# Performance work log

Measured on AMD Instinct MI355X. Metric: run time of the kernel, lower is better.

## Reference

```python
import jax, jax.numpy as jnp
import numpy as np
import math

B, T, C, H = 16384, 64, 48, 48


def setup_inputs() -> dict:
    key = jax.random.key(0)
    kx, kq, kk, kv = jax.random.split(key, 4)
    return {
        "x": jax.random.normal(kx, (B, T, C), dtype=jnp.float32),
        "Wq": jax.random.normal(kq, (C, H), dtype=jnp.float32) * 0.02,
        "Wk": jax.random.normal(kk, (C, H), dtype=jnp.float32) * 0.02,
        "Wv": jax.random.normal(kv, (C, H), dtype=jnp.float32) * 0.02,
    }


def reference(x, Wq, Wk, Wv):
    # x: [B, T, C]; projections (Linear with bias=False): [B, T, H]
    q = x @ Wq
    k = x @ Wk
    v = x @ Wv
    scale = 1.0 / math.sqrt(H)
    # scores: [B, T, T]
    wei = jnp.einsum("bth,bsh->bts", q, k) * scale
    causal = jnp.tril(jnp.ones((T, T), dtype=bool))  # tril mask, T==BLOCK_SIZE
    wei = jnp.where(causal, wei, -jnp.inf)
    wei = jax.nn.softmax(wei, axis=-1)
    # dropout is identity in eval mode
    return jnp.einsum("bts,bsh->bth", wei, v)
```

## Files before the change

kernel.cpp:

```cpp
#include <hip/hip_runtime.h>
#include <math.h>

typedef __bf16 bf16x8 __attribute__((ext_vector_type(8)));
typedef float f32x4 __attribute__((ext_vector_type(4)));
typedef unsigned short u16;

__device__ __forceinline__ u16 f2b(float f) {
  unsigned u = __builtin_bit_cast(unsigned, f);
  u = (u + 0x7fffu + ((u >> 16) & 1u)) >> 16;
  return (u16)u;
}

__device__ __forceinline__ f32x4 mfma16(bf16x8 a, bf16x8 b, f32x4 c) {
  return __builtin_amdgcn_mfma_f32_16x16x32_bf16(a, b, c, 0, 0, 0);
}

__device__ __forceinline__ int sw(int r, int c) {
  return (r << 6) + ((((c >> 3) ^ r) & 7) << 3) + (c & 7);
}
__device__ __forceinline__ int swc(int r, int ch) {
  return (r << 6) + (((ch ^ r) & 7) << 3);
}

__global__ __launch_bounds__(256) void head_prep(const float* __restrict__ Wq,
                                                 const float* __restrict__ Wk,
                                                 const float* __restrict__ Wv,
                                                 u16* __restrict__ ws) {
  __shared__ float wq[2304], wk[2304], wv[2304];
  const float scale = 0.14433756729740643f;
  for (int i = threadIdx.x; i < 2304; i += 256) {
    wq[i] = Wq[i];
    wk[i] = Wk[i];
    wv[i] = Wv[i];
  }
  __syncthreads();
  for (int idx = threadIdx.x; idx < 96 * 64; idx += 256) {
    int r = idx >> 6, c = idx & 63;
    float v = 0.f;
    if (c < 48) {
      if (r < 48) {
        float a = 0.f;
        for (int h = 0; h < 48; ++h) a += wq[c * 48 + h] * wk[r * 48 + h];
        v = a * scale;
      } else {
        v = wv[c * 48 + (r - 48)];
      }
    }
    ws[sw(r, c)] = f2b(v);
  }
}

__global__ __launch_bounds__(256, 6) void head_main(const float* __restrict__ x,
                                                    const u16* __restrict__ wimg,
                                                    float* __restrict__ out) {
  __shared__ u16 lds[208 * 64];
  u16* const R0 = lds;
  u16* const X  = lds + 96 * 64;
  u16* const VT = lds + 160 * 64;

  const int tid  = threadIdx.x;
  const int lane = tid & 63;
  const int w    = tid >> 6;
  const int qd   = lane >> 4;
  const int col  = lane & 15;
  const long b   = blockIdx.x;

  {
    const uint4* src = (const uint4*)wimg;
    uint4* dst = (uint4*)lds;
    dst[tid]       = src[tid];
    dst[tid + 256] = src[tid + 256];
    dst[tid + 512] = src[tid + 512];
  }
  {
    const float* xb = x + b * 3072;
#pragma unroll
    for (int it = 0; it < 3; ++it) {
      int flat = tid * 4 + it * 1024;
      float4 v = *(const float4*)(xb + flat);
      int row = flat / 48;
      int c0  = flat % 48;
      ushort4 pk;
      pk.x = f2b(v.x); pk.y = f2b(v.y); pk.z = f2b(v.z); pk.w = f2b(v.w);
      *(ushort4*)(X + sw(row, c0)) = pk;
    }
    int zr = tid >> 2;
    int zq = tid & 3;
    ushort4 z = {0, 0, 0, 0};
    *(ushort4*)(X + swc(zr, 6 + (zq >> 1)) + (zq & 1) * 4) = z;
  }
  __syncthreads();

  f32x4 aq[3];
  {
    const int ar = 16 * w + col;
    const bf16x8 xa0 = *(const bf16x8*)(X + swc(ar, qd));
    const bf16x8 xa1 = *(const bf16x8*)(X + swc(ar, qd + 4));
    const u16* WM = R0;
    const u16* WV = R0 + 48 * 64;
#pragma unroll
    for (int n = 0; n < 3; ++n) {
      const int br = 16 * n + col;
      const int b0 = swc(br, qd);
      const int b1 = swc(br, qd + 4);
      f32x4 av = {0.f, 0.f, 0.f, 0.f};
      av = mfma16(xa0, *(const bf16x8*)(WV + b0), av);
      av = mfma16(xa1, *(const bf16x8*)(WV + b1), av);
      f32x4 a = {0.f, 0.f, 0.f, 0.f};
      a = mfma16(xa0, *(const bf16x8*)(WM + b0), a);
      a = mfma16(xa1, *(const bf16x8*)(WM + b1), a);
      aq[n] = a;
      ushort4 pv;
      pv.x = f2b(av[0]); pv.y = f2b(av[1]); pv.z = f2b(av[2]); pv.w = f2b(av[3]);
      *(ushort4*)(VT + sw(16 * n + col, 16 * w + qd * 4)) = pv;
    }
  }
  __syncthreads();

#pragma unroll
  for (int n = 0; n < 3; ++n)
#pragma unroll
    for (int i = 0; i < 4; ++i)
      R0[sw(16 * w + qd * 4 + i, 16 * n + col)] = f2b(aq[n][i]);
  __threadfence_block();

  float sv[4][4];
  {
    const int ar = 16 * w + col;
    const bf16x8 qa0 = *(const bf16x8*)(R0 + swc(ar, qd));
    const bf16x8 qa1 = *(const bf16x8*)(R0 + swc(ar, qd + 4));
#pragma unroll
    for (int st = 0; st < 4; ++st) {
      const int br = 16 * st + col;
      f32x4 a = {0.f, 0.f, 0.f, 0.f};
      a = mfma16(qa0, *(const bf16x8*)(X + swc(br, qd)), a);
      a = mfma16(qa1, *(const bf16x8*)(X + swc(br, qd + 4)), a);
#pragma unroll
      for (int i = 0; i < 4; ++i) sv[st][i] = a[i];
    }
  }

  float m4[4] = {-INFINITY, -INFINITY, -INFINITY, -INFINITY};
#pragma unroll
  for (int st = 0; st < 4; ++st)
#pragma unroll
    for (int i = 0; i < 4; ++i) {
      int tg = 16 * w + qd * 4 + i;
      int sg = 16 * st + col;
      float v = (sg <= tg) ? sv[st][i] : -INFINITY;
      sv[st][i] = v;
      m4[i] = fmaxf(m4[i], v);
    }
#pragma unroll
  for (int d = 1; d < 16; d <<= 1)
#pragma unroll
    for (int i = 0; i < 4; ++i) m4[i] = fmaxf(m4[i], __shfl_xor(m4[i], d, 64));
  float l4[4] = {0.f, 0.f, 0.f, 0.f};
#pragma unroll
  for (int st = 0; st < 4; ++st)
#pragma unroll
    for (int i = 0; i < 4; ++i) {
      float p = __expf(sv[st][i] - m4[i]);
      sv[st][i] = p;
      l4[i] += p;
    }
#pragma unroll
  for (int d = 1; d < 16; d <<= 1)
#pragma unroll
    for (int i = 0; i < 4; ++i) l4[i] += __shfl_xor(l4[i], d, 64);

  __syncthreads();

#pragma unroll
  for (int st = 0; st < 4; ++st)
#pragma unroll
    for (int i = 0; i < 4; ++i)
      X[sw(16 * w + qd * 4 + i, 16 * st + col)] = f2b(sv[st][i]);
  __threadfence_block();

  f32x4 o0 = {0.f, 0.f, 0.f, 0.f}, o1 = o0, o2 = o0;
  {
    const int pr = 16 * w + col;
#pragma unroll
    for (int kt = 0; kt < 2; ++kt) {
      const int ch = qd + 4 * kt;
      bf16x8 pa = *(const bf16x8*)(X + swc(pr, ch));
      o0 = mfma16(pa, *(const bf16x8*)(VT + swc(0  + col, ch)), o0);
      o1 = mfma16(pa, *(const bf16x8*)(VT + swc(16 + col, ch)), o1);
      o2 = mfma16(pa, *(const bf16x8*)(VT + swc(32 + col, ch)), o2);
    }
  }
  float rl[4];
#pragma unroll
  for (int i = 0; i < 4; ++i) rl[i] = __builtin_amdgcn_rcpf(l4[i]);

  float* ob = out + b * 3072 + (16 * w + qd * 4) * 48 + col;
#pragma unroll
  for (int i = 0; i < 4; ++i) {
    ob[i * 48 +  0] = o0[i] * rl[i];
    ob[i * 48 + 16] = o1[i] * rl[i];
    ob[i * 48 + 32] = o2[i] * rl[i];
  }
}

extern "C" void kernel_launch(void* const* d_in, const int* in_sizes, int n_in,
                              void* d_out, int out_size, void* d_ws, size_t ws_size,
                              hipStream_t stream) {
  const float* x  = (const float*)d_in[0];
  const float* Wq = (const float*)d_in[1];
  const float* Wk = (const float*)d_in[2];
  const float* Wv = (const float*)d_in[3];
  u16* wimg = (u16*)d_ws;
  head_prep<<<1, 256, 0, stream>>>(Wq, Wk, Wv, wimg);
  head_main<<<16384, 256, 0, stream>>>(x, wimg, (float*)d_out);
}
```

Baseline: 340.6 us.

## Process several batches per block with register prefetch of next x tile

Each block now handles NB=8 consecutive batch elements in a loop. The weight image is loaded into LDS once per block instead of once per batch element, and the next batch's x tile is prefetched into registers while the current one is computed. This is meant to amortise the weight load and launch overhead and to hide global-load latency. In exchange, each block uses more LDS because Q and X get separate buffers, occupancy is lowered to 4 blocks per SM, and the grid shrinks to 2048 blocks.

Result: slower. 357.3 us (+4.9%).

```diff
diff --git a/kernel.cpp b/kernel.cpp
--- a/kernel.cpp
+++ b/kernel.cpp
@@ -4,6 +4,8 @@
 typedef __bf16 bf16x8 __attribute__((ext_vector_type(8)));
 typedef float f32x4 __attribute__((ext_vector_type(4)));
 typedef unsigned short u16;
+
+#define NB 8
 
 __device__ __forceinline__ u16 f2b(float f) {
   unsigned u = __builtin_bit_cast(unsigned, f);
@@ -50,20 +52,21 @@
   }
 }
 
-__global__ __launch_bounds__(256, 6) void head_main(const float* __restrict__ x,
+__global__ __launch_bounds__(256, 4) void head_main(const float* __restrict__ x,
                                                     const u16* __restrict__ wimg,
                                                     float* __restrict__ out) {
-  __shared__ u16 lds[208 * 64];
-  u16* const R0 = lds;
-  u16* const X  = lds + 96 * 64;
-  u16* const VT = lds + 160 * 64;
+  __shared__ u16 lds[272 * 64];
+  u16* const W  = lds;
+  u16* const QM = lds + 96 * 64;
+  u16* const X  = lds + 160 * 64;
+  u16* const VT = lds + 224 * 64;
 
   const int tid  = threadIdx.x;
   const int lane = tid & 63;
   const int w    = tid >> 6;
   const int qd   = lane >> 4;
   const int col  = lane & 15;
-  const long b   = blockIdx.x;
+  const long b0  = (long)blockIdx.x * NB;
 
   {
     const uint4* src = (const uint4*)wimg;
@@ -73,133 +76,155 @@
     dst[tid + 512] = src[tid + 512];
   }
   {
-    const float* xb = x + b * 3072;
-#pragma unroll
-    for (int it = 0; it < 3; ++it) {
-      int flat = tid * 4 + it * 1024;
-      float4 v = *(const float4*)(xb + flat);
-      int row = flat / 48;
-      int c0  = flat % 48;
-      ushort4 pk;
-      pk.x = f2b(v.x); pk.y = f2b(v.y); pk.z = f2b(v.z); pk.w = f2b(v.w);
-      *(ushort4*)(X + sw(row, c0)) = pk;
-    }
-    int zr = tid >> 2;
-    int zq = tid & 3;
     ushort4 z = {0, 0, 0, 0};
-    *(ushort4*)(X + swc(zr, 6 + (zq >> 1)) + (zq & 1) * 4) = z;
-  }
-  __syncthreads();
-
-  f32x4 aq[3];
-  {
-    const int ar = 16 * w + col;
-    const bf16x8 xa0 = *(const bf16x8*)(X + swc(ar, qd));
-    const bf16x8 xa1 = *(const bf16x8*)(X + swc(ar, qd + 4));
-    const u16* WM = R0;
-    const u16* WV = R0 + 48 * 64;
-#pragma unroll
-    for (int n = 0; n < 3; ++n) {
-      const int br = 16 * n + col;
-      const int b0 = swc(br, qd);
-      const int b1 = swc(br, qd + 4);
-      f32x4 av = {0.f, 0.f, 0.f, 0.f};
-      av = mfma16(xa0, *(const bf16x8*)(WV + b0), av);
-      av = mfma16(xa1, *(const bf16x8*)(WV + b1), av);
-      f32x4 a = {0.f, 0.f, 0.f, 0.f};
-      a = mfma16(xa0, *(const bf16x8*)(WM + b0), a);
-      a = mfma16(xa1, *(const bf16x8*)(WM + b1), a);
-      aq[n] = a;
-      ushort4 pv;
-      pv.x = f2b(av[0]); pv.y = f2b(av[1]); pv.z = f2b(av[2]); pv.w = f2b(av[3]);
-      *(ushort4*)(VT + sw(16 * n + col, 16 * w + qd * 4)) = pv;
-    }
-  }
-  __syncthreads();
-
-#pragma unroll
-  for (int n = 0; n < 3; ++n)
-#pragma unroll
-    for (int i = 0; i < 4; ++i)
-      R0[sw(16 * w + qd * 4 + i, 16 * n + col)] = f2b(aq[n][i]);
-  __threadfence_block();
-
-  float sv[4][4];
-  {
-    const int ar = 16 * w + col;
-    const bf16x8 qa0 = *(const bf16x8*)(R0 + swc(ar, qd));
-    const bf16x8 qa1 = *(const bf16x8*)(R0 + swc(ar, qd + 4));
-#pragma unroll
-    for (int st = 0; st < 4; ++st) {
-      const int br = 16 * st + col;
-      f32x4 a = {0.f, 0.f, 0.f, 0.f};
-      a = mfma16(qa0, *(const bf16x8*)(X + swc(br, qd)), a);
-      a = mfma16(qa1, *(const bf16x8*)(X + swc(br, qd + 4)), a);
-#pragma unroll
-      for (int i = 0; i < 4; ++i) sv[st][i] = a[i];
-    }
-  }
-
-  float m4[4] = {-INFINITY, -INFINITY, -INFINITY, -INFINITY};
-#pragma unroll
-  for (int st = 0; st < 4; ++st)
-#pragma unroll
-    for (int i = 0; i < 4; ++i) {
-      int tg = 16 * w + qd * 4 + i;
-      int sg = 16 * st + col;
-      float v = (sg <= tg) ? sv[st][i] : -INFINITY;
-      sv[st][i] = v;
-      m4[i] = fmaxf(m4[i], v);
-    }
-#pragma unroll
-  for (int d = 1; d < 16; d <<= 1)
-#pragma unroll
-    for (int i = 0; i < 4; ++i) m4[i] = fmaxf(m4[i], __shfl_xor(m4[i], d, 64));
-  float l4[4] = {0.f, 0.f, 0.f, 0.f};
-#pragma unroll
-  for (int st = 0; st < 4; ++st)
-#pragma unroll
-    for (int i = 0; i < 4; ++i) {
-      float p = __expf(sv[st][i] - m4[i]);
-      sv[st][i] = p;
-      l4[i] += p;
-    }
-#pragma unroll
-  for (int d = 1; d < 16; d <<= 1)
-#pragma unroll
-    for (int i = 0; i < 4; ++i) l4[i] += __shfl_xor(l4[i], d, 64);
-
-  __syncthreads();
-
-#pragma unroll
-  for (int st = 0; st < 4; ++st)
-#pragma unroll
-    for (int i = 0; i < 4; ++i)
-      X[sw(16 * w + qd * 4 + i, 16 * st + col)] = f2b(sv[st][i]);
-  __threadfence_block();
-
-  f32x4 o0 = {0.f, 0.f, 0.f, 0.f}, o1 = o0, o2 = o0;
-  {
-    const int pr = 16 * w + col;
-#pragma unroll
-    for (int kt = 0; kt < 2; ++kt) {
-      const int ch = qd + 4 * kt;
-      bf16x8 pa = *(const bf16x8*)(X + swc(pr, ch));
-      o0 = mfma16(pa, *(const bf16x8*)(VT + swc(0  + col, ch)), o0);
-      o1 = mfma16(pa, *(const bf16x8*)(VT + swc(16 + col, ch)), o1);
-      o2 = mfma16(pa, *(const bf16x8*)(VT + swc(32 + col, ch)), o2);
-    }
-  }
-  float rl[4];
-#pragma unroll
-  for (int i = 0; i < 4; ++i) rl[i] = __builtin_amdgcn_rcpf(l4[i]);
-
-  float* ob = out + b * 3072 + (16 * w + qd * 4) * 48 + col;
-#pragma unroll
-  for (int i = 0; i < 4; ++i) {
-    ob[i * 48 +  0] = o0[i] * rl[i];
-    ob[i * 48 + 16] = o1[i] * rl[i];
-    ob[i * 48 + 32] = o2[i] * rl[i];
+    int zr = tid >> 2, zq = tid & 3;
+    *(ushort4*)(QM + swc(zr, 6 + (zq >> 1)) + (zq & 1) * 4) = z;
+  }
+
+  const int f0 = tid * 4, f1 = f0 + 1024, f2 = f0 + 2048;
+  const int xw0 = sw(f0 / 48, f0 % 48);
+  const int xw1 = sw(f1 / 48, f1 % 48);
+  const int xw2 = sw(f2 / 48, f2 % 48);
+  const int zr = tid >> 2, zq = tid & 3;
+  const int zpad = swc(zr, 6 + (zq >> 1)) + (zq & 1) * 4;
+
+  const int ar = 16 * w + col;
+  const int a0 = swc(ar, qd), a1 = swc(ar, qd + 4);
+
+  const float* xb = x + b0 * 3072;
+  float4 p0 = *(const float4*)(xb + f0);
+  float4 p1 = *(const float4*)(xb + f1);
+  float4 p2 = *(const float4*)(xb + f2);
+
+  for (int i = 0; i < NB; ++i) {
+    if (i > 0) __syncthreads();
+
+    {
+      ushort4 s;
+      s.x = f2b(p0.x); s.y = f2b(p0.y); s.z = f2b(p0.z); s.w = f2b(p0.w);
+      *(ushort4*)(X + xw0) = s;
+      s.x = f2b(p1.x); s.y = f2b(p1.y); s.z = f2b(p1.z); s.w = f2b(p1.w);
+      *(ushort4*)(X + xw1) = s;
+      s.x = f2b(p2.x); s.y = f2b(p2.y); s.z = f2b(p2.z); s.w = f2b(p2.w);
+      *(ushort4*)(X + xw2) = s;
+      ushort4 z = {0, 0, 0, 0};
+      *(ushort4*)(X + zpad) = z;
+    }
+    {
+      const long bn = b0 + ((i < NB - 1) ? i + 1 : i);
+      const float* xn = x + bn * 3072;
+      p0 = *(const float4*)(xn + f0);
+      p1 = *(const float4*)(xn + f1);
+      p2 = *(const float4*)(xn + f2);
+    }
+    __syncthreads();
+
+    f32x4 aq[3];
+    {
+      const bf16x8 xa0 = *(const bf16x8*)(X + a0);
+      const bf16x8 xa1 = *(const bf16x8*)(X + a1);
+      const u16* WM = W;
+      const u16* WV = W + 48 * 64;
+#pragma unroll
+      for (int n = 0; n < 3; ++n) {
+        const int br = 16 * n + col;
+        const int c0 = swc(br, qd), c1 = swc(br, qd + 4);
+        f32x4 av = {0.f, 0.f, 0.f, 0.f};
+        av = mfma16(xa0, *(const bf16x8*)(WV + c0), av);
+        av = mfma16(xa1, *(const bf16x8*)(WV + c1), av);
+        f32x4 a = {0.f, 0.f, 0.f, 0.f};
+        a = mfma16(xa0, *(const bf16x8*)(WM + c0), a);
+        a = mfma16(xa1, *(const bf16x8*)(WM + c1), a);
+        aq[n] = a;
+        ushort4 pv;
+        pv.x = f2b(av[0]); pv.y = f2b(av[1]); pv.z = f2b(av[2]); pv.w = f2b(av[3]);
+        *(ushort4*)(VT + sw(16 * n + col, 16 * w + qd * 4)) = pv;
+      }
+    }
+
+#pragma unroll
+    for (int n = 0; n < 3; ++n)
+#pragma unroll
+      for (int j = 0; j < 4; ++j)
+        QM[sw(16 * w + qd * 4 + j, 16 * n + col)] = f2b(aq[n][j]);
+    __threadfence_block();
+
+    float sv[4][4];
+    {
+      const bf16x8 qa0 = *(const bf16x8*)(QM + a0);
+      const bf16x8 qa1 = *(const bf16x8*)(QM + a1);
+#pragma unroll
+      for (int st = 0; st < 4; ++st) {
+        const int br = 16 * st + col;
+        f32x4 a = {0.f, 0.f, 0.f, 0.f};
+        a = mfma16(qa0, *(const bf16x8*)(X + swc(br, qd)), a);
+        a = mfma16(qa1, *(const bf16x8*)(X + swc(br, qd + 4)), a);
+#pragma unroll
+        for (int j = 0; j < 4; ++j) sv[st][j] = a[j];
+      }
+    }
+
+    float m4[4] = {-INFINITY, -INFINITY, -INFINITY, -INFINITY};
+#pragma unroll
+    for (int st = 0; st < 4; ++st)
+#pragma unroll
+      for (int j = 0; j < 4; ++j) {
+        int tg = 16 * w + qd * 4 + j;
+        int sg = 16 * st + col;
+        float v = (sg <= tg) ? sv[st][j] : -INFINITY;
+        sv[st][j] = v;
+        m4[j] = fmaxf(m4[j], v);
+      }
+#pragma unroll
+    for (int d = 1; d < 16; d <<= 1)
+#pragma unroll
+      for (int j = 0; j < 4; ++j) m4[j] = fmaxf(m4[j], __shfl_xor(m4[j], d, 64));
+    float l4[4] = {0.f, 0.f, 0.f, 0.f};
+#pragma unroll
+    for (int st = 0; st < 4; ++st)
+#pragma unroll
+      for (int j = 0; j < 4; ++j) {
+        float p = __expf(sv[st][j] - m4[j]);
+        sv[st][j] = p;
+        l4[j] += p;
+      }
+#pragma unroll
+    for (int d = 1; d < 16; d <<= 1)
+#pragma unroll
+      for (int j = 0; j < 4; ++j) l4[j] += __shfl_xor(l4[j], d, 64);
+
+    __syncthreads();
+
+#pragma unroll
+    for (int st = 0; st < 4; ++st)
+#pragma unroll
+      for (int j = 0; j < 4; ++j)
+        X[sw(16 * w + qd * 4 + j, 16 * st + col)] = f2b(sv[st][j]);
+    __threadfence_block();
+
+    f32x4 o0 = {0.f, 0.f, 0.f, 0.f}, o1 = o0, o2 = o0;
+    {
+      const int pr = 16 * w + col;
+#pragma unroll
+      for (int kt = 0; kt < 2; ++kt) {
+        const int ch = qd + 4 * kt;
+        bf16x8 pa = *(const bf16x8*)(X + swc(pr, ch));
+        o0 = mfma16(pa, *(const bf16x8*)(VT + swc(0  + col, ch)), o0);
+        o1 = mfma16(pa, *(const bf16x8*)(VT + swc(16 + col, ch)), o1);
+        o2 = mfma16(pa, *(const bf16x8*)(VT + swc(32 + col, ch)), o2);
+      }
+    }
+    float rl[4];
+#pragma unroll
+    for (int j = 0; j < 4; ++j) rl[j] = __builtin_amdgcn_rcpf(l4[j]);
+
+    float* ob = out + (b0 + i) * 3072 + (16 * w + qd * 4) * 48 + col;
+#pragma unroll
+    for (int j = 0; j < 4; ++j) {
+      ob[j * 48 +  0] = o0[j] * rl[j];
+      ob[j * 48 + 16] = o1[j] * rl[j];
+      ob[j * 48 + 32] = o2[j] * rl[j];
+    }
   }
 }
 
@@ -212,5 +237,5 @@
   const float* Wv = (const float*)d_in[3];
   u16* wimg = (u16*)d_ws;
   head_prep<<<1, 256, 0, stream>>>(Wq, Wk, Wv, wimg);
-  head_main<<<16384, 256, 0, stream>>>(x, wimg, (float*)d_out);
-}
+  head_main<<<16384 / NB, 256, 0, stream>>>(x, wimg, (float*)d_out);
+}
```
